# Optimization experiments

Measured on AMD Instinct MI355X. Metric: run time of the kernel, lower is better.

The kernel has to match this reference:

```python
import jax, jax.numpy as jnp
import numpy as np

N_QUBITS = 12
DEPTH = 4
OUT_DIM = 4096
BATCH = 2048
M_IN = 4096


def setup_inputs() -> dict:
    key = jax.random.key(0)
    k1, k2 = jax.random.split(key)
    x = jax.random.normal(k1, (BATCH, M_IN), dtype=jnp.float32)
    w = jax.random.uniform(k2, (DEPTH, N_QUBITS, 3), dtype=jnp.float32) * (2.0 * np.pi)
    return {"x": x, "w": w}


def _rot_matrix(phi, theta, omega):
    # PennyLane Rot(phi, theta, omega) = RZ(omega) @ RY(theta) @ RZ(phi)
    c = jnp.cos(theta / 2)
    s = jnp.sin(theta / 2)
    m = jnp.stack([
        jnp.stack([jnp.exp(-1j * (phi + omega) / 2) * c, -jnp.exp(1j * (phi - omega) / 2) * s]),
        jnp.stack([jnp.exp(-1j * (phi - omega) / 2) * s, jnp.exp(1j * (phi + omega) / 2) * c]),
    ])
    return m.astype(jnp.complex64)


def _apply_1q(s, U, q):
    # s: (B,) + (2,)*n ; wire q lives on axis q+1 (wire 0 = MSB, default.qubit order)
    s = jnp.moveaxis(s, q + 1, -1)
    s = jnp.einsum('...j,ij->...i', s, U)
    return jnp.moveaxis(s, -1, q + 1)


def _cnot(s, c, t):
    # control wire c < target wire t; flip target axis on the control=1 slice
    p0 = s[(slice(None),) * (c + 1) + (0,)]
    p1 = jnp.flip(s[(slice(None),) * (c + 1) + (1,)], axis=t)  # axis t after removing axis c+1
    return jnp.stack([p0, p1], axis=c + 1)


def _layer(s, wl):
    n = N_QUBITS
    for i in range(n):
        s = _apply_1q(s, _rot_matrix(wl[i, 0], wl[i, 1], wl[i, 2]), i)
    for i in range(n):
        for j in range(i + 1, n):
            s = _cnot(s, i, j)
    return s


def reference(x, w):
    B, m = x.shape
    n = N_QUBITS
    # amplitude embedding: per-sample L2 normalize with uniform fallback
    norm = jnp.linalg.norm(x, axis=1, keepdims=True)
    ok = norm > 1e-10
    amp = jnp.where(ok, x / jnp.where(ok, norm, 1.0), 1.0 / np.sqrt(m))
    s = amp.astype(jnp.complex64).reshape((B,) + (2,) * n)
    for layer in range(DEPTH):
        s = _layer(s, w[layer])
    sv = s.reshape(B, -1)
    probs = sv.real ** 2 + sv.imag ** 2
    pn = probs[:, :OUT_DIM]
    tot = jnp.sum(pn, axis=1, keepdims=True)
    okp = tot > 1e-10
    out = jnp.where(okp, pn / jnp.where(okp, tot, 1.0), 1.0 / OUT_DIM)
    return out.astype(x.dtype)
```

## Files before the change

### kernel.cpp

```cpp
#include <hip/hip_runtime.h>
#include <math.h>

#define NQ 12
#define DIM 4096
#define NLAYER 4
#define NT 512

typedef float v2 __attribute__((ext_vector_type(2)));
typedef float v4f __attribute__((ext_vector_type(4)));

__device__ __forceinline__ v2 sp(float a) { v2 r; r.x = a; r.y = a; return r; }
__device__ __forceinline__ v2 pkfma(v2 a, float b, v2 c) {
  return __builtin_elementwise_fma(a, sp(b), c);
}

#define CFENCE asm volatile("" ::: "memory")

constexpr int sfun_c(int z) { z ^= z >> 1; z ^= z >> 2; z ^= z >> 4; z ^= z >> 8; return z & (DIM - 1); }
__device__ __forceinline__ int sfun_d(int z) { z ^= z >> 1; z ^= z >> 2; z ^= z >> 4; z ^= z >> 8; return z & (DIM - 1); }
constexpr int swz_c(int z) {
  const int b0 = ((z >> 5) ^ (z >> 6)) & 1;
  const int b1 = ((z >> 4) ^ (z >> 7)) & 1;
  const int b2 = ((z >> 3) ^ (z >> 5) ^ (z >> 8)) & 1;
  return z ^ b0 ^ (b1 << 1) ^ (b2 << 2);
}
__device__ __forceinline__ int swz_d(int z) {
  const int b0 = ((z >> 5) ^ (z >> 6)) & 1;
  const int b1 = ((z >> 4) ^ (z >> 7)) & 1;
  const int b2 = ((z >> 3) ^ (z >> 5) ^ (z >> 8)) & 1;
  return z ^ b0 ^ (b1 << 1) ^ (b2 << 2);
}

struct KT { int A[8], B[8], C[8], D[8], G[8]; };
constexpr KT mkKT() {
  KT k{};
  for (int j = 0; j < 8; ++j) {
    k.A[j] = swz_c(j << 9) << 4;
    k.B[j] = swz_c(j << 6) << 4;
    k.C[j] = swz_c(j << 3) << 4;
    k.D[j] = swz_c(j) << 4;
    k.G[j] = swz_c(sfun_c(j << 9)) << 4;
  }
  return k;
}
constexpr KT KTab = mkKT();

__device__ __forceinline__ v2 block_reduce_sum2(v2 v, v2* red) {
  const int tid = threadIdx.x;
#pragma unroll
  for (int off = 32; off > 0; off >>= 1) {
    v.x += __shfl_down(v.x, off, 64);
    v.y += __shfl_down(v.y, off, 64);
  }
  if ((tid & 63) == 0) red[tid >> 6] = v;
  __syncthreads();
  if (tid == 0) {
    v2 s = sp(0.f);
#pragma unroll
    for (int i = 0; i < NT / 64; ++i) s += red[i];
    red[0] = s;
  }
  __syncthreads();
  v2 r = red[0];
  __syncthreads();
  return r;
}

__device__ __forceinline__ void apply_pair(v4f& A, v4f& B, const v4f g0, const v4f g1) {
  const v2 ar = A.lo, ai = A.hi, br = B.lo, bi = B.hi;
  const v2 nr0 = pkfma(bi, -g0.w, pkfma(br, g0.z, pkfma(ai, -g0.y, ar * sp(g0.x))));
  const v2 ni0 = pkfma(br,  g0.w, pkfma(bi, g0.z, pkfma(ar,  g0.y, ai * sp(g0.x))));
  const v2 nr1 = pkfma(bi, -g1.w, pkfma(br, g1.z, pkfma(ai, -g1.y, ar * sp(g1.x))));
  const v2 ni1 = pkfma(br,  g1.w, pkfma(bi, g1.z, pkfma(ar,  g1.y, ai * sp(g1.x))));
  A.lo = nr0; A.hi = ni0; B.lo = nr1; B.hi = ni1;
}

template <int RT>
__device__ __forceinline__ void gates3(v4f s[8], const float* __restrict__ GW) {
#pragma unroll
  for (int i = 0; i < 3; ++i) {
    const int q = 2 + 3 * RT - i;
    const v4f g0 = *(const v4f*)(GW + q * 8);
    const v4f g1 = *(const v4f*)(GW + q * 8 + 4);
#pragma unroll
    for (int pe = 0; pe < 4; ++pe) {
      const int e0 = ((pe >> i) << (i + 1)) | (pe & ((1 << i) - 1));
      apply_pair(s[e0], s[e0 | (1 << i)], g0, g1);
    }
  }
}

#define LOAD8(ADDR)                                       \
  _Pragma("unroll")                                       \
  for (int j = 0; j < 8; ++j)                             \
    s[j] = *(const v4f*)(st + ADDR[j]);
#define STORE8(ADDR)                                      \
  _Pragma("unroll")                                       \
  for (int j = 0; j < 8; ++j)                             \
    *(v4f*)(st + ADDR[j]) = s[j];

__global__ void prep_gates(const float* __restrict__ w, float* __restrict__ gw) {
  const int t = threadIdx.x;
  if (t < NLAYER * NQ) {
    const float* wp = w + t * 3;
    float phi = wp[0], th = wp[1], om = wp[2];
    float sn, cc, sa, ca, sb, cb;
    sincosf(0.5f * th, &sn, &cc);
    sincosf(0.5f * (phi + om), &sa, &ca);
    sincosf(0.5f * (phi - om), &sb, &cb);
    float* g = gw + t * 8;
    g[0] = ca * cc;  g[1] = -sa * cc;
    g[2] = -cb * sn; g[3] = -sb * sn;
    g[4] = cb * sn;  g[5] = -sb * sn;
    g[6] = ca * cc;  g[7] = sa * cc;
  }
}

__global__ __launch_bounds__(NT, 4) void qsim_kernel(
    const float* __restrict__ x, const float* __restrict__ gw,
    float* __restrict__ out) {
  extern __shared__ __align__(16) char smem[];
  char* st  = smem;
  v2*   red = (v2*)(smem + DIM * 16);

  const int t = threadIdx.x;
  const int lane = t & 63, wave = t >> 6;
  const long r0 = 2L * blockIdx.x;

  const float4* xa = (const float4*)(x + r0 * DIM) + t * 2;
  const float4* xb = (const float4*)(x + (r0 + 1) * DIM) + t * 2;
  const float4 a0 = xa[0], a1 = xa[1], b0 = xb[0], b1 = xb[1];
  const float va[8] = {a0.x, a0.y, a0.z, a0.w, a1.x, a1.y, a1.z, a1.w};
  const float vb[8] = {b0.x, b0.y, b0.z, b0.w, b1.x, b1.y, b1.z, b1.w};
  v2 ss = sp(0.f);
#pragma unroll
  for (int e = 0; e < 8; ++e) { ss.x += va[e] * va[e]; ss.y += vb[e] * vb[e]; }
  const v2 nsq = block_reduce_sum2(ss, red);
  const float n0 = sqrtf(nsq.x), n1 = sqrtf(nsq.y);
  const bool ok0 = n0 > 1e-10f, ok1 = n1 > 1e-10f;
  const float i0f = ok0 ? 1.0f / n0 : 0.f, i1f = ok1 ? 1.0f / n1 : 0.f;

  const int baseAb = swz_d(wave | (lane << 3)) << 4;
  const int baseBb = swz_d(wave | ((lane & 7) << 3) | ((lane >> 3) << 9)) << 4;
  const int baseCb = swz_d(wave | (lane << 6)) << 4;
  const int baseDb = swz_d((lane << 3) | (wave << 9)) << 4;
  const int baseGb = swz_d(sfun_d(wave | (lane << 3))) << 4;
  const int baseOb = swz_d(sfun_d(t)) << 4;
  int aA[8], aB[8], aC[8], aD[8], aG[8];
#pragma unroll
  for (int j = 0; j < 8; ++j) {
    aA[j] = baseAb ^ KTab.A[j];
    aB[j] = baseBb ^ KTab.B[j];
    aC[j] = baseCb ^ KTab.C[j];
    aD[j] = baseDb ^ KTab.D[j];
    aG[j] = baseGb ^ KTab.G[j];
  }

#pragma unroll
  for (int e = 0; e < 8; ++e) {
    v4f u;
    u.x = ok0 ? va[e] * i0f : 0.015625f;
    u.y = ok1 ? vb[e] * i1f : 0.015625f;
    u.z = 0.f; u.w = 0.f;
    *(v4f*)(st + aD[e]) = u;
  }
  __syncthreads();

  v4f s[8];
#pragma unroll
  for (int L = 0; L < NLAYER; ++L) {
    const float* GW = gw + L * (NQ * 8);

    if (L == 0) {
      LOAD8(aA)
      gates3<0>(s, GW);
      STORE8(aA)
    } else {
      LOAD8(aG)
      gates3<0>(s, GW);
      __syncthreads();
      STORE8(aA)
    }
    CFENCE;
    LOAD8(aB)
    gates3<1>(s, GW);
    STORE8(aB)
    CFENCE;
    LOAD8(aC)
    gates3<2>(s, GW);
    STORE8(aC)
    __syncthreads();
    LOAD8(aD)
    gates3<3>(s, GW);
    STORE8(aD)
    __syncthreads();
  }

  float q0[8], q1[8];
  v2 ps = sp(0.f);
#pragma unroll
  for (int k = 0; k < 8; ++k) {
    const v4f v = *(const v4f*)(st + (baseOb ^ KTab.G[k]));
    q0[k] = v.x * v.x + v.z * v.z;
    q1[k] = v.y * v.y + v.w * v.w;
    ps.x += q0[k]; ps.y += q1[k];
  }
  const v2 tot = block_reduce_sum2(ps, red);
  const bool k0 = tot.x > 1e-10f, k1 = tot.y > 1e-10f;
  const float t0 = k0 ? 1.0f / tot.x : 0.f, t1 = k1 ? 1.0f / tot.y : 0.f;
  float* o0 = out + r0 * DIM;
  float* o1 = out + (r0 + 1) * DIM;
#pragma unroll
  for (int k = 0; k < 8; ++k) {
    o0[t + k * NT] = k0 ? q0[k] * t0 : (1.0f / DIM);
    o1[t + k * NT] = k1 ? q1[k] * t1 : (1.0f / DIM);
  }
}

extern "C" void kernel_launch(void* const* d_in, const int* in_sizes, int n_in,
                              void* d_out, int out_size, void* d_ws, size_t ws_size,
                              hipStream_t stream) {
  const float* x = (const float*)d_in[0];
  const float* w = (const float*)d_in[1];
  float* out = (float*)d_out;
  float* gw = (float*)d_ws;
  const int B = in_sizes[0] / DIM;
  prep_gates<<<1, 64, 0, stream>>>(w, gw);
  const size_t smem = DIM * 16 + (NT / 64) * sizeof(v2);
  qsim_kernel<<<B / 2, NT, smem, stream>>>(x, gw, out);
}
```

Baseline: 78.26 us.

## Apply three qubit gates via DPP lane exchange to drop one LDS round trip

```diff
diff --git a/kernel.cpp b/kernel.cpp
--- a/kernel.cpp
+++ b/kernel.cpp
@@ -31,15 +31,14 @@
   return z ^ b0 ^ (b1 << 1) ^ (b2 << 2);
 }
 
-struct KT { int A[8], B[8], C[8], D[8], G[8]; };
+struct KT { int P1[8], P2[8], P3[8], G[8]; };
 constexpr KT mkKT() {
   KT k{};
   for (int j = 0; j < 8; ++j) {
-    k.A[j] = swz_c(j << 9) << 4;
-    k.B[j] = swz_c(j << 6) << 4;
-    k.C[j] = swz_c(j << 3) << 4;
-    k.D[j] = swz_c(j) << 4;
-    k.G[j] = swz_c(sfun_c(j << 9)) << 4;
+    k.P1[j] = swz_c(j << 9) << 4;
+    k.P2[j] = swz_c(((j & 1) << 5) | (((j >> 1) & 1) << 7) | (((j >> 2) & 1) << 8)) << 4;
+    k.P3[j] = swz_c(j) << 4;
+    k.G[j]  = swz_c(sfun_c(j << 9)) << 4;
   }
   return k;
 }
@@ -75,18 +74,41 @@
   A.lo = nr0; A.hi = ni0; B.lo = nr1; B.hi = ni1;
 }
 
-template <int RT>
-__device__ __forceinline__ void gates3(v4f s[8], const float* __restrict__ GW) {
+template <int Q0, int Q1, int Q2>
+__device__ __forceinline__ void gatesR(v4f s[8], const float* __restrict__ GW) {
+  constexpr int Q[3] = {Q0, Q1, Q2};
 #pragma unroll
   for (int i = 0; i < 3; ++i) {
-    const int q = 2 + 3 * RT - i;
-    const v4f g0 = *(const v4f*)(GW + q * 8);
-    const v4f g1 = *(const v4f*)(GW + q * 8 + 4);
+    const v4f g0 = *(const v4f*)(GW + Q[i] * 8);
+    const v4f g1 = *(const v4f*)(GW + Q[i] * 8 + 4);
 #pragma unroll
     for (int pe = 0; pe < 4; ++pe) {
       const int e0 = ((pe >> i) << (i + 1)) | (pe & ((1 << i) - 1));
       apply_pair(s[e0], s[e0 | (1 << i)], g0, g1);
     }
+  }
+}
+
+template <int CTRL>
+__device__ __forceinline__ float dppx(float v) {
+  return __builtin_bit_cast(float, __builtin_amdgcn_update_dpp(
+      0, __builtin_bit_cast(int, v), CTRL, 0xF, 0xF, true));
+}
+
+template <int CTRL, int BITMASK>
+__device__ __forceinline__ void dppgate(v4f s[8], const float* __restrict__ g,
+                                        const int lane) {
+  const bool r = (lane & BITMASK) != 0;
+  const float cSx = r ? g[6] : g[0], cSy = r ? g[7] : g[1];
+  const float cPx = r ? g[4] : g[2], cPy = r ? g[5] : g[3];
+#pragma unroll
+  for (int j = 0; j < 8; ++j) {
+    const v2 re = s[j].lo, im = s[j].hi;
+    v2 pre, pim;
+    pre.x = dppx<CTRL>(re.x); pre.y = dppx<CTRL>(re.y);
+    pim.x = dppx<CTRL>(im.x); pim.y = dppx<CTRL>(im.y);
+    s[j].lo = pkfma(pim, -cPy, pkfma(pre, cPx, pkfma(im, -cSy, re * sp(cSx))));
+    s[j].hi = pkfma(pre,  cPy, pkfma(pim, cPx, pkfma(re,  cSy, im * sp(cSx))));
   }
 }
 
@@ -140,20 +162,19 @@
   const bool ok0 = n0 > 1e-10f, ok1 = n1 > 1e-10f;
   const float i0f = ok0 ? 1.0f / n0 : 0.f, i1f = ok1 ? 1.0f / n1 : 0.f;
 
-  const int baseAb = swz_d(wave | (lane << 3)) << 4;
-  const int baseBb = swz_d(wave | ((lane & 7) << 3) | ((lane >> 3) << 9)) << 4;
-  const int baseCb = swz_d(wave | (lane << 6)) << 4;
-  const int baseDb = swz_d((lane << 3) | (wave << 9)) << 4;
-  const int baseGb = swz_d(sfun_d(wave | (lane << 3))) << 4;
-  const int baseOb = swz_d(sfun_d(t)) << 4;
-  int aA[8], aB[8], aC[8], aD[8], aG[8];
+  const int baseP1 = swz_d(wave | (lane << 3)) << 4;
+  const int baseP2 = swz_d(wave | ((lane & 3) << 3) | (((lane >> 2) & 1) << 6)
+                           | ((lane >> 3) << 9)) << 4;
+  const int baseP3 = swz_d((lane << 3) | (wave << 9)) << 4;
+  const int baseG  = swz_d(sfun_d(wave | (lane << 3))) << 4;
+  const int baseO  = swz_d(sfun_d(t)) << 4;
+  int aP1[8], aP2[8], aP3[8], aG[8];
 #pragma unroll
   for (int j = 0; j < 8; ++j) {
-    aA[j] = baseAb ^ KTab.A[j];
-    aB[j] = baseBb ^ KTab.B[j];
-    aC[j] = baseCb ^ KTab.C[j];
-    aD[j] = baseDb ^ KTab.D[j];
-    aG[j] = baseGb ^ KTab.G[j];
+    aP1[j] = baseP1 ^ KTab.P1[j];
+    aP2[j] = baseP2 ^ KTab.P2[j];
+    aP3[j] = baseP3 ^ KTab.P3[j];
+    aG[j]  = baseG ^ KTab.G[j];
   }
 
 #pragma unroll
@@ -162,7 +183,7 @@
     u.x = ok0 ? va[e] * i0f : 0.015625f;
     u.y = ok1 ? vb[e] * i1f : 0.015625f;
     u.z = 0.f; u.w = 0.f;
-    *(v4f*)(st + aD[e]) = u;
+    *(v4f*)(st + aP3[e]) = u;
   }
   __syncthreads();
 
@@ -172,27 +193,24 @@
     const float* GW = gw + L * (NQ * 8);
 
     if (L == 0) {
-      LOAD8(aA)
-      gates3<0>(s, GW);
-      STORE8(aA)
+      LOAD8(aP1)
     } else {
       LOAD8(aG)
-      gates3<0>(s, GW);
-      __syncthreads();
-      STORE8(aA)
     }
+    gatesR<2, 1, 0>(s, GW);
+    dppgate<0xB1, 1>(s, GW + 8 * 8, lane);
+    dppgate<0x4E, 2>(s, GW + 7 * 8, lane);
+    dppgate<0x128, 8>(s, GW + 5 * 8, lane);
+    if (L > 0) __syncthreads();
+    STORE8(aP1)
     CFENCE;
-    LOAD8(aB)
-    gates3<1>(s, GW);
-    STORE8(aB)
-    CFENCE;
-    LOAD8(aC)
-    gates3<2>(s, GW);
-    STORE8(aC)
+    LOAD8(aP2)
+    gatesR<6, 4, 3>(s, GW);
+    STORE8(aP2)
     __syncthreads();
-    LOAD8(aD)
-    gates3<3>(s, GW);
-    STORE8(aD)
+    LOAD8(aP3)
+    gatesR<11, 10, 9>(s, GW);
+    STORE8(aP3)
     __syncthreads();
   }
 
@@ -200,7 +218,7 @@
   v2 ps = sp(0.f);
 #pragma unroll
   for (int k = 0; k < 8; ++k) {
-    const v4f v = *(const v4f*)(st + (baseOb ^ KTab.G[k]));
+    const v4f v = *(const v4f*)(st + (baseO ^ KTab.G[k]));
     q0[k] = v.x * v.x + v.z * v.z;
     q1[k] = v.y * v.y + v.w * v.w;
     ps.x += q0[k]; ps.y += q1[k];
```

Result: slower. 81.79 us (+4.5%).
